# Kernel tuning notes

Hardware: AMD Instinct MI355X
Metric: run time of the kernel (lower is better)

The kernel has to match this reference:

```python
import jax, jax.numpy as jnp
import numpy as np

DIM = 768
H = 12          # num_heads
KV = 4          # kv_heads
D = DIM // H    # head_dim = 64
ROPE_BASE = 10000.0
WINDOW = 8
B, N = 4, 1024


def setup_inputs() -> dict:
    key = jax.random.key(0)
    ks = jax.random.split(key, 8)
    s = 0.02  # weight scale for sane magnitudes
    return {
        "x": jax.random.normal(ks[0], (B, N, DIM), jnp.float32),
        "Wq": jax.random.normal(ks[1], (2 * DIM, DIM), jnp.float32) * s,
        "Wk": jax.random.normal(ks[2], (2 * DIM * KV // H, DIM), jnp.float32) * s,
        "Wv1": jax.random.normal(ks[3], (DIM * KV // H, DIM), jnp.float32) * s,
        "Wv2": jax.random.normal(ks[4], (DIM * KV // H, DIM), jnp.float32) * s,
        "lambda_p": jnp.full((H, 1, 1), -2.0, jnp.float32),
        "Wo": jax.random.normal(ks[5], (DIM, DIM), jnp.float32) * s,
        "bo": jax.random.normal(ks[6], (DIM,), jnp.float32) * s,
    }


def _rotate_half(x):
    x1 = x[..., ::2]
    x2 = x[..., 1::2]
    return jnp.stack([-x2, x1], axis=-1).reshape(x.shape)


def _rope_cos_sin(n, dtype):
    side = int(n ** 0.5)
    if side * side == n:
        h = np.arange(side, dtype=np.float32)
        gh, gw = np.meshgrid(h, h, indexing="ij")
        pos_h, pos_w = gh.reshape(-1), gw.reshape(-1)
    else:
        pos_h = np.arange(n, dtype=np.float32)
        pos_w = np.zeros_like(pos_h)
    dim_half = D // 2
    inv_freq = ROPE_BASE ** (-np.arange(dim_half, dtype=np.float32) / dim_half)
    theta = np.concatenate([pos_h[:, None] * inv_freq[None, :],
                            pos_w[:, None] * inv_freq[None, :]], axis=1)  # [N, D]
    cos = jnp.asarray(np.cos(theta), dtype)[None, None]  # [1,1,N,D]
    sin = jnp.asarray(np.sin(theta), dtype)[None, None]
    return cos, sin


def _apply_rope(q, cos, sin):
    return q * cos + _rotate_half(q) * sin


def _qk_norm(t):
    return t / (jnp.linalg.norm(t, axis=-1, keepdims=True) + 1e-6)


def _window_mask(n, dtype):
    side = int(n ** 0.5)
    if side * side == n:
        h = np.arange(side)
        gh, gw = np.meshgrid(h, h, indexing="ij")
        coords = np.stack([gh.reshape(-1), gw.reshape(-1)], axis=1)  # [N,2]
        dist = np.abs(coords[:, None, :] - coords[None, :, :]).max(-1)  # Chebyshev
    else:
        idx = np.arange(n)
        dist = np.abs(idx[None, :] - idx[:, None])
    return jnp.asarray(np.where(dist > WINDOW, -np.inf, 0.0).astype(np.float32), dtype)


def _attend(q, k, v, mask):
    # q,k,v: [B,H,N,D]; mask additive [N,N]
    scale = 1.0 / np.sqrt(D)
    scores = jnp.einsum("bhnd,bhmd->bhnm", q, k) * scale + mask
    return jnp.einsum("bhnm,bhmd->bhnd", jax.nn.softmax(scores, axis=-1), v)


def reference(x, Wq, Wk, Wv1, Wv2, lambda_p, Wo, bo):
    b, n, c = x.shape
    rep = H // KV
    q = (x @ Wq.T).reshape(b, n, 2, H, D).transpose(2, 0, 3, 1, 4)   # [2,B,H,N,D]
    k = (x @ Wk.T).reshape(b, n, 2, KV, D).transpose(2, 0, 3, 1, 4)  # [2,B,KV,N,D]
    v1 = (x @ Wv1.T).reshape(b, n, KV, D).transpose(0, 2, 1, 3)      # [B,KV,N,D]
    v2 = (x @ Wv2.T).reshape(b, n, KV, D).transpose(0, 2, 1, 3)
    q1, q2 = q[0], q[1]
    k1, k2 = k[0], k[1]
    # GQA: repeat_interleave over head axis
    k1 = jnp.repeat(k1, rep, axis=1)
    k2 = jnp.repeat(k2, rep, axis=1)
    v1 = jnp.repeat(v1, rep, axis=1)
    v2 = jnp.repeat(v2, rep, axis=1)
    cos, sin = _rope_cos_sin(n, x.dtype)
    q1, q2 = _apply_rope(q1, cos, sin), _apply_rope(q2, cos, sin)
    k1, k2 = _apply_rope(k1, cos, sin), _apply_rope(k2, cos, sin)
    q1, q2, k1, k2 = _qk_norm(q1), _qk_norm(q2), _qk_norm(k1), _qk_norm(k2)
    mask = _window_mask(n, x.dtype)
    out1 = _attend(q1, k1, v1, mask)
    out2 = _attend(q2, k2, v2, mask)
    lam = jax.nn.softplus(lambda_p)  # [H,1,1] broadcasts over [B,H,N,D]
    out = out1 - lam[None] * out2
    out = out.transpose(0, 2, 1, 3).reshape(b, n, c)
    return out @ Wo.T + bo
```

## Files before the change

kernel.cpp:

```cpp
#include <hip/hip_runtime.h>
#include <hip/hip_bf16.h>

#define BATCH 4
#define NSEQ  1024
#define DIM   768
#define NH    12
#define NKV   4
#define HD    64
#define NTOK  (BATCH*NSEQ)

using bf16 = __hip_bfloat16;
typedef __attribute__((ext_vector_type(8))) short short8;
typedef __attribute__((ext_vector_type(4))) float floatx4;
typedef __attribute__((ext_vector_type(4))) unsigned uint4v;

__device__ __forceinline__ float b2f(short x) {
  unsigned u = ((unsigned)(unsigned short)x) << 16;
  return __builtin_bit_cast(float, u);
}
__device__ __forceinline__ unsigned short f2b(float f) {
  unsigned u = __builtin_bit_cast(unsigned, f);
  unsigned r = u + 0x7FFF + ((u >> 16) & 1);
  return (unsigned short)(r >> 16);
}
__device__ __forceinline__ unsigned cvtpk(float lo, float hi) {
  unsigned r;
  asm("v_cvt_pk_bf16_f32 %0, %1, %2" : "=v"(r) : "v"(lo), "v"(hi));
  return r;
}

__device__ __forceinline__ void load_lds_16(const bf16* g, bf16* l) {
  __builtin_amdgcn_global_load_lds(
      (const __attribute__((address_space(1))) void*)g,
      (__attribute__((address_space(3))) void*)l, 16, 0, 0);
}

__global__ __launch_bounds__(256) void cvt_all(
    const float* __restrict__ x,  const float* __restrict__ wq,
    const float* __restrict__ wk, const float* __restrict__ wv1,
    const float* __restrict__ wv2, const float* __restrict__ wo,
    bf16* __restrict__ xb,  bf16* __restrict__ wqb, bf16* __restrict__ wkb,
    bf16* __restrict__ wv1b, bf16* __restrict__ wv2b, bf16* __restrict__ wob)
{
  int i = blockIdx.x * 256 + threadIdx.x;
  const float* s; bf16* d; int off;
  if      (i <  786432) { s = x;   d = xb;   off = i; }
  else if (i < 1081344) { s = wq;  d = wqb;  off = i -  786432; }
  else if (i < 1179648) { s = wk;  d = wkb;  off = i - 1081344; }
  else if (i < 1228800) { s = wv1; d = wv1b; off = i - 1179648; }
  else if (i < 1277952) { s = wv2; d = wv2b; off = i - 1228800; }
  else                  { s = wo;  d = wob;  off = i - 1277952; }
  float4 f = reinterpret_cast<const float4*>(s)[off];
  ushort4 u;
  u.x = f2b(f.x); u.y = f2b(f.y); u.z = f2b(f.z); u.w = f2b(f.w);
  reinterpret_cast<ushort4*>(d)[off] = u;
}

__global__ __launch_bounds__(256, 2) void gemm_qkv(
    const bf16* __restrict__ xb,
    const bf16* __restrict__ Wqb, const bf16* __restrict__ Wkb,
    const bf16* __restrict__ Wv1b, const bf16* __restrict__ Wv2b,
    bf16* __restrict__ Qpk, bf16* __restrict__ Kpk,
    bf16* __restrict__ Vpk1, bf16* __restrict__ Vpk2)
{
  __shared__ __align__(16) bf16 As[128 * 64];
  __shared__ __align__(16) bf16 Ws[128 * 64];

  const int bn = blockIdx.x, bm = blockIdx.y;
  const bf16* Wp;
  if (bn < 12)      Wp = Wqb  + (size_t)bn * 128 * 768;
  else if (bn < 16) Wp = Wkb  + (size_t)(bn - 12) * 128 * 768;
  else if (bn < 18) Wp = Wv1b + (size_t)(bn - 16) * 128 * 768;
  else              Wp = Wv2b + (size_t)(bn - 18) * 128 * 768;

  const int t = threadIdx.x, wave = t >> 6, lane = t & 63;
  const int wm = wave >> 1, wn = wave & 1;
  const int quad = lane >> 4, lr = lane & 15;

  const int srow = wave * 32 + (lane >> 3);
  const int scol = ((lane & 7) ^ (lane >> 3)) * 8;
  const bf16* Ag = xb + (size_t)(bm * 128 + srow) * 768 + scol;
  const bf16* Wg = Wp + (size_t)srow * 768 + scol;
  bf16* Al = As + wave * 32 * 64;
  bf16* Wl = Ws + wave * 32 * 64;

  floatx4 acc[4][4] = {};

  for (int k0 = 0; k0 < 768; k0 += 64) {
    #pragma unroll
    for (int c = 0; c < 4; ++c) {
      load_lds_16(Ag + (size_t)c * 8 * 768 + k0, Al + c * 8 * 64);
      load_lds_16(Wg + (size_t)c * 8 * 768 + k0, Wl + c * 8 * 64);
    }
    __syncthreads();

    short8 af[4][2], wf[4][2];
    #pragma unroll
    for (int mt = 0; mt < 4; ++mt)
      #pragma unroll
      for (int ks = 0; ks < 2; ++ks)
        af[mt][ks] = *reinterpret_cast<const short8*>(
            &As[(wm * 64 + mt * 16 + lr) * 64 + ((ks * 32 + quad * 8) ^ ((lr & 7) * 8))]);
    #pragma unroll
    for (int nt = 0; nt < 4; ++nt)
      #pragma unroll
      for (int ks = 0; ks < 2; ++ks)
        wf[nt][ks] = *reinterpret_cast<const short8*>(
            &Ws[(wn * 64 + nt * 16 + lr) * 64 + ((ks * 32 + quad * 8) ^ ((lr & 7) * 8))]);

    #pragma unroll
    for (int mt = 0; mt < 4; ++mt)
      #pragma unroll
      for (int nt = 0; nt < 4; ++nt) {
        acc[mt][nt] = __builtin_amdgcn_mfma_f32_16x16x32_bf16(af[mt][0], wf[nt][0], acc[mt][nt], 0, 0, 0);
        acc[mt][nt] = __builtin_amdgcn_mfma_f32_16x16x32_bf16(af[mt][1], wf[nt][1], acc[mt][nt], 0, 0, 0);
      }
    __syncthreads();
  }

  if (bn < 16) {
    const float K2 = 0.41524101186098309f;
    const float invf0 = exp2f(-(float)lr * K2);
    const float invf1 = exp2f(-(float)(16 + lr) * K2);
    const float sgn = (lr & 1) ? 1.f : -1.f;
    const bool isq = (bn < 12);
    const int hq = bn * 2 + wn;
    const int sq_ = hq / 12, hq_ = hq % 12;
    const int hh = (bn - 12) * 2 + wn;
    const int sk_ = hh >> 2, kvh_ = hh & 3;
    const int qk128 = (lr >> 3) * 128;
    #pragma unroll
    for (int mt = 0; mt < 4; ++mt) {
      const int row0 = bm * 128 + wm * 64 + mt * 16 + quad * 4;
      const int n0 = row0 & (NSEQ - 1);
      const int bb = row0 >> 10, kh = n0 >> 5;
      const float ph = (float)kh;
      const float pw0 = (float)(n0 & 31);
      const float t0 = ph * invf0, t1 = ph * invf1;
      const float c0 = __cosf(t0), s0 = __sinf(t0);
      const float c1 = __cosf(t1), s1 = __sinf(t1);
      bf16* tb0;
      if (isq) {
        tb0 = Qpk + ((size_t)((bb * 2 + sq_) * 12 + hq_) * 32 + kh) * 2048
              + (size_t)(mt & 1) * 1024 + qk128 + (quad * 4) * 8 + (lr & 7);
      } else {
        tb0 = Kpk + ((size_t)((bb * 2 + sk_) * 4 + kvh_) * 32 + kh) * 2048
              + (size_t)(mt & 1) * 1024 + qk128 + (quad * 4) * 8 + (lr & 7);
      }
      #pragma unroll
      for (int r = 0; r < 4; ++r) {
        float v0 = acc[mt][0][r];
        float v1 = acc[mt][1][r];
        float v2 = acc[mt][2][r];
        float v3 = acc[mt][3][r];
        float rot0 = sgn * __shfl_xor(v0, 1);
        float rot1 = sgn * __shfl_xor(v1, 1);
        float rot2 = sgn * __shfl_xor(v2, 1);
        float rot3 = sgn * __shfl_xor(v3, 1);
        float pw = pw0 + (float)r;
        float t2 = pw * invf0, t3 = pw * invf1;
        float rv0 = v0 * c0 + rot0 * s0;
        float rv1 = v1 * c1 + rot1 * s1;
        float rv2 = v2 * __cosf(t2) + rot2 * __sinf(t2);
        float rv3 = v3 * __cosf(t3) + rot3 * __sinf(t3);
        float ss = rv0 * rv0 + rv1 * rv1 + rv2 * rv2 + rv3 * rv3;
        #pragma unroll
        for (int off = 1; off < 16; off <<= 1) ss += __shfl_xor(ss, off);
        float sc = 1.f / (sqrtf(ss) + 1e-6f);
        if (isq) sc *= 0.18033688011112042f;
        bf16* tb = tb0 + r * 8;
        unsigned pkA = cvtpk(rv0 * sc, rv1 * sc);
        unsigned pkB = cvtpk(rv2 * sc, rv3 * sc);
        *(unsigned short*)&tb[0]   = (unsigned short)pkA;
        *(unsigned short*)&tb[256] = (unsigned short)(pkA >> 16);
        *(unsigned short*)&tb[512] = (unsigned short)pkB;
        *(unsigned short*)&tb[768] = (unsigned short)(pkB >> 16);
      }
    }
  } else {
    const bool is2 = (bn >= 18);
    bf16* Vp = is2 ? Vpk2 : Vpk1;
    const int kvh_ = (bn - (is2 ? 18 : 16)) * 2 + wn;
    #pragma unroll
    for (int mt = 0; mt < 4; ++mt)
      #pragma unroll
      for (int r = 0; r < 4; ++r) {
        int row = bm * 128 + wm * 64 + mt * 16 + quad * 4 + r;
        int n = row & (NSEQ - 1);
        int bb = row >> 10, kh = n >> 5;
        int rowm = (mt & 1) * 16 + quad * 4 + r;
        int quad_v = rowm >> 3, j = rowm & 7;
        bf16* tb = Vp + ((size_t)(bb * 4 + kvh_) * 32 + kh) * 2048
                   + quad_v * 128 + lr * 8 + j;
        unsigned pkA = cvtpk(acc[mt][0][r], acc[mt][1][r]);
        unsigned pkB = cvtpk(acc[mt][2][r], acc[mt][3][r]);
        *(unsigned short*)&tb[0]    = (unsigned short)pkA;
        *(unsigned short*)&tb[512]  = (unsigned short)(pkA >> 16);
        *(unsigned short*)&tb[1024] = (unsigned short)pkB;
        *(unsigned short*)&tb[1536] = (unsigned short)(pkB >> 16);
      }
  }
}

__global__ __launch_bounds__(256) void gemm_out(
    const bf16* __restrict__ Xb, const bf16* __restrict__ Wob,
    float* __restrict__ out, const float* __restrict__ bias)
{
  __shared__ __align__(16) bf16 As[64 * 64];
  __shared__ __align__(16) bf16 Ws[64 * 64];

  const int bn = blockIdx.x, bm = blockIdx.y;
  const int t = threadIdx.x, wave = t >> 6, lane = t & 63;
  const int wm = wave >> 1, wn = wave & 1;
  const int quad = lane >> 4, lr = lane & 15;

  const int srow = wave * 16 + (lane >> 3);
  const int scol = ((lane & 7) ^ (lane >> 3)) * 8;
  const bf16* Ag = Xb  + (size_t)(bm * 64 + srow) * 768 + scol;
  const bf16* Wg = Wob + (size_t)(bn * 64 + srow) * 768 + scol;
  bf16* Al = As + wave * 16 * 64;
  bf16* Wl = Ws + wave * 16 * 64;

  floatx4 acc[2][2] = {};

  for (int k0 = 0; k0 < 768; k0 += 64) {
    #pragma unroll
    for (int c = 0; c < 2; ++c) {
      load_lds_16(Ag + (size_t)c * 8 * 768 + k0, Al + c * 8 * 64);
      load_lds_16(Wg + (size_t)c * 8 * 768 + k0, Wl + c * 8 * 64);
    }
    __syncthreads();

    short8 af[2][2], wf[2][2];
    #pragma unroll
    for (int mt = 0; mt < 2; ++mt)
      #pragma unroll
      for (int ks = 0; ks < 2; ++ks)
        af[mt][ks] = *reinterpret_cast<const short8*>(
            &As[(wm * 32 + mt * 16 + lr) * 64 + ((ks * 32 + quad * 8) ^ ((lr & 7) * 8))]);
    #pragma unroll
    for (int nt = 0; nt < 2; ++nt)
      #pragma unroll
      for (int ks = 0; ks < 2; ++ks)
        wf[nt][ks] = *reinterpret_cast<const short8*>(
            &Ws[(wn * 32 + nt * 16 + lr) * 64 + ((ks * 32 + quad * 8) ^ ((lr & 7) * 8))]);

    #pragma unroll
    for (int mt = 0; mt < 2; ++mt)
      #pragma unroll
      for (int nt = 0; nt < 2; ++nt) {
        acc[mt][nt] = __builtin_amdgcn_mfma_f32_16x16x32_bf16(af[mt][0], wf[nt][0], acc[mt][nt], 0, 0, 0);
        acc[mt][nt] = __builtin_amdgcn_mfma_f32_16x16x32_bf16(af[mt][1], wf[nt][1], acc[mt][nt], 0, 0, 0);
      }
    __syncthreads();
  }

  #pragma unroll
  for (int nt = 0; nt < 2; ++nt) {
    int col = bn * 64 + wn * 32 + nt * 16 + lr;
    float bv = bias[col];
    #pragma unroll
    for (int mt = 0; mt < 2; ++mt)
      #pragma unroll
      for (int r = 0; r < 4; ++r) {
        int row = bm * 64 + wm * 32 + mt * 16 + quad * 4 + r;
        out[(size_t)row * 768 + col] = acc[mt][nt][r] + bv;
      }
  }
}

struct Frag { short8 kf[2][2]; short8 vf[4]; };

__device__ __forceinline__ void attn_load(
    Frag& f, const bf16* __restrict__ kp, const bf16* __restrict__ vp,
    int kh, int lane8)
{
  const bf16* kt = kp + (size_t)kh * 2048 + lane8;
  const bf16* vt = vp + (size_t)kh * 2048 + lane8;
  f.kf[0][0] = *reinterpret_cast<const short8*>(kt);
  f.kf[0][1] = *reinterpret_cast<const short8*>(kt + 512);
  f.kf[1][0] = *reinterpret_cast<const short8*>(kt + 1024);
  f.kf[1][1] = *reinterpret_cast<const short8*>(kt + 1536);
  f.vf[0] = *reinterpret_cast<const short8*>(vt);
  f.vf[1] = *reinterpret_cast<const short8*>(vt + 512);
  f.vf[2] = *reinterpret_cast<const short8*>(vt + 1024);
  f.vf[3] = *reinterpret_cast<const short8*>(vt + 1536);
}

__device__ __forceinline__ void attn_step(
    const short8 (&qf)[2][2], const Frag& f, unsigned maskbits,
    floatx4 (&O)[2][4], float (&psum)[2], int quad)
{
  floatx4 St[2][2] = {};
  #pragma unroll
  for (int ks = 0; ks < 2; ++ks) {
    St[0][0] = __builtin_amdgcn_mfma_f32_16x16x32_bf16(f.kf[0][ks], qf[0][ks], St[0][0], 0, 0, 0);
    St[0][1] = __builtin_amdgcn_mfma_f32_16x16x32_bf16(f.kf[0][ks], qf[1][ks], St[0][1], 0, 0, 0);
    St[1][0] = __builtin_amdgcn_mfma_f32_16x16x32_bf16(f.kf[1][ks], qf[0][ks], St[1][0], 0, 0, 0);
    St[1][1] = __builtin_amdgcn_mfma_f32_16x16x32_bf16(f.kf[1][ks], qf[1][ks], St[1][1], 0, 0, 0);
  }

  unsigned pk[2][2][2];
  #pragma unroll
  for (int kt = 0; kt < 2; ++kt)
    #pragma unroll
    for (int mt = 0; mt < 2; ++mt) {
      float pr[4];
      #pragma unroll
      for (int r = 0; r < 4; ++r) {
        float p = __builtin_amdgcn_exp2f(St[kt][mt][r]);
        p = ((maskbits >> (kt * 8 + mt * 4 + r)) & 1u) ? p : 0.0f;
        psum[mt] += p;
        pr[r] = p;
      }
      pk[kt][mt][0] = cvtpk(pr[0], pr[1]);
      pk[kt][mt][1] = cvtpk(pr[2], pr[3]);
    }

  const bool oddq = (quad & 1);
  #pragma unroll
  for (int mt = 0; mt < 2; ++mt) {
    uint4v regs;
    #pragma unroll
    for (int h = 0; h < 2; ++h) {
      unsigned a = pk[0][mt][h], b = pk[1][mt][h];
      asm("v_permlane32_swap_b32 %0, %1" : "+v"(a), "+v"(b));
      unsigned sa = (unsigned)__shfl_xor((int)a, 16);
      unsigned sb = (unsigned)__shfl_xor((int)b, 16);
      regs[0 + h] = oddq ? sb : a;
      regs[2 + h] = oddq ? b  : sa;
    }
    short8 pa = __builtin_bit_cast(short8, regs);
    #pragma unroll
    for (int ntd = 0; ntd < 4; ++ntd)
      O[mt][ntd] = __builtin_amdgcn_mfma_f32_16x16x32_bf16(pa, f.vf[ntd], O[mt][ntd], 0, 0, 0);
  }
}

__global__ __launch_bounds__(256, 2) void attn_mfma(
    const bf16* __restrict__ Qpk, const bf16* __restrict__ Kpk,
    const bf16* __restrict__ Vpk1, const bf16* __restrict__ Vpk2,
    const float* __restrict__ lambda_p, bf16* __restrict__ X)
{
  __shared__ __align__(16) char smem[20480];

  const int bid = blockIdx.x;
  const int qh = bid & 31;
  const int hb = bid >> 5;
  const int h  = hb % 12;
  const int b  = hb / 12;
  const int kvh = h / 3;

  const int t = threadIdx.x;
  const int w = t >> 6;
  const int s = w >> 1;
  const int half = w & 1;
  const int lane = t & 63;
  const int quad = lane >> 4, lr = lane & 15;
  const int lane8 = lane * 8;

  float* myO = (float*)(smem + (s ? 10240 : 0));
  float* myP = (float*)(smem + (s ? 10240 : 0) + 8192);
  bf16* Xs = (bf16*)smem;

  const int tok0 = b * NSEQ + qh * 32;

  short8 qf[2][2];
  {
    const bf16* qt = Qpk + ((size_t)((b * 2 + s) * 12 + h) * 32 + qh) * 2048 + lane8;
    qf[0][0] = *reinterpret_cast<const short8*>(qt);
    qf[0][1] = *reinterpret_cast<const short8*>(qt + 512);
    qf[1][0] = *reinterpret_cast<const short8*>(qt + 1024);
    qf[1][1] = *reinterpret_cast<const short8*>(qt + 1536);
  }

  unsigned maskbits = 0;
  #pragma unroll
  for (int kt = 0; kt < 2; ++kt)
    #pragma unroll
    for (int mt = 0; mt < 2; ++mt)
      #pragma unroll
      for (int r = 0; r < 4; ++r) {
        int wk = kt * 16 + quad * 4 + r;
        int wq = mt * 16 + lr;
        int d = wk - wq; if (d < 0) d = -d;
        if (d <= 8) maskbits |= 1u << (kt * 8 + mt * 4 + r);
      }

  floatx4 O[2][4] = {};
  float psum[2] = {};

  const int kh0 = (qh > 8) ? qh - 8 : 0;
  const int kh1 = (qh < 23) ? qh + 8 : 31;
  const int cnt = kh1 - kh0 + 1;
  const int cA = (cnt + 1) >> 1;
  const int khA = half ? kh0 + cA : kh0;
  const int khB = half ? kh1 : kh0 + cA - 1;

  const bf16* kpbase = Kpk + (size_t)((b * 2 + s) * 4 + kvh) * 32 * 2048;
  const bf16* vpbase = (s ? Vpk2 : Vpk1) + (size_t)(b * 4 + kvh) * 32 * 2048;

  Frag fA, fB;
  attn_load(fA, kpbase, vpbase, khA, lane8);
  attn_load(fB, kpbase, vpbase, (khA + 1 <= khB) ? khA + 1 : khB, lane8);

  int i = khA;
  while (true) {
    attn_step(qf, fA, maskbits, O, psum, quad);
    if (i == khB) break;
    ++i;
    attn_load(fA, kpbase, vpbase, (i + 1 <= khB) ? i + 1 : i, lane8);
    attn_step(qf, fB, maskbits, O, psum, quad);
    if (i == khB) break;
    ++i;
    attn_load(fB, kpbase, vpbase, (i + 1 <= khB) ? i + 1 : i, lane8);
  }

  auto writeslab = [&]() {
    #pragma unroll
    for (int mt = 0; mt < 2; ++mt)
      #pragma unroll
      for (int ntd = 0; ntd < 4; ++ntd)
        *reinterpret_cast<floatx4*>(&myO[(mt * 4 + ntd) * 256 + lane * 4]) = O[mt][ntd];
    myP[lane]      = psum[0];
    myP[64 + lane] = psum[1];
  };
  auto readadd_norm = [&]() {
    #pragma unroll
    for (int mt = 0; mt < 2; ++mt)
      #pragma unroll
      for (int ntd = 0; ntd < 4; ++ntd)
        O[mt][ntd] += *reinterpret_cast<const floatx4*>(&myO[(mt * 4 + ntd) * 256 + lane * 4]);
    psum[0] += myP[lane];
    psum[1] += myP[64 + lane];
    #pragma unroll
    for (int mt = 0; mt < 2; ++mt) {
      psum[mt] += __shfl_xor(psum[mt], 16);
      psum[mt] += __shfl_xor(psum[mt], 32);
      psum[mt] = 1.f / psum[mt];
    }
    #pragma unroll
    for (int mt = 0; mt < 2; ++mt) {
      float invq[4];
      #pragma unroll
      for (int r = 0; r < 4; ++r)
        invq[r] = __shfl(psum[mt], (lane & 48) + quad * 4 + r);
      #pragma unroll
      for (int ntd = 0; ntd < 4; ++ntd)
        #pragma unroll
        for (int r = 0; r < 4; ++r)
          O[mt][ntd][r] *= invq[r];
    }
  };

  __syncthreads();
  if (half) writeslab();
  __syncthreads();
  if (!half) {
    readadd_norm();
    if (s) {
      #pragma unroll
      for (int mt = 0; mt < 2; ++mt)
        #pragma unroll
        for (int ntd = 0; ntd < 4; ++ntd)
          *reinterpret_cast<floatx4*>(&myO[(mt * 4 + ntd) * 256 + lane * 4]) = O[mt][ntd];
    }
  }
  __syncthreads();
  if (w == 0) {
    const float* O2s = (const float*)(smem + 10240);
    float lam = log1pf(__expf(lambda_p[h]));
    #pragma unroll
    for (int mt = 0; mt < 2; ++mt)
      #pragma unroll
      for (int ntd = 0; ntd < 4; ++ntd) {
        floatx4 o2 = *reinterpret_cast<const floatx4*>(&O2s[(mt * 4 + ntd) * 256 + lane * 4]);
        #pragma unroll
        for (int r = 0; r < 4; ++r) {
          float xv = O[mt][ntd][r] - lam * o2[r];
          *(unsigned short*)&Xs[(mt * 16 + quad * 4 + r) * 72 + ntd * 16 + lr] = f2b(xv);
        }
      }
  }
  __syncthreads();

  {
    int row = t >> 3, seg = t & 7;
    short8 xv = *reinterpret_cast<const short8*>(&Xs[row * 72 + seg * 8]);
    *reinterpret_cast<short8*>(X + (size_t)(tok0 + row) * 768 + h * 64 + seg * 8) = xv;
  }
}

extern "C" void kernel_launch(void* const* d_in, const int* in_sizes, int n_in,
                              void* d_out, int out_size, void* d_ws, size_t ws_size,
                              hipStream_t stream)
{
  const float* x        = (const float*)d_in[0];
  const float* Wq       = (const float*)d_in[1];
  const float* Wk       = (const float*)d_in[2];
  const float* Wv1      = (const float*)d_in[3];
  const float* Wv2      = (const float*)d_in[4];
  const float* lambda_p = (const float*)d_in[5];
  const float* Wo       = (const float*)d_in[6];
  const float* bo       = (const float*)d_in[7];
  float* out = (float*)d_out;

  bf16* xb   = (bf16*)d_ws;
  bf16* Wqb  = xb   + (size_t)NTOK * 768;
  bf16* Wkb  = Wqb  + (size_t)1536 * 768;
  bf16* Wv1b = Wkb  + (size_t)512 * 768;
  bf16* Wv2b = Wv1b + (size_t)256 * 768;
  bf16* Wob  = Wv2b + (size_t)256 * 768;
  bf16* Qpk  = Wob  + (size_t)768 * 768;
  bf16* Xb   = Qpk  + (size_t)NTOK * 1536;
  bf16* Vpk1 = Xb   + (size_t)NTOK * 768;
  bf16* Vpk2 = Vpk1 + (size_t)512 * 2048;
  bf16* Kpk  = Vpk2 + (size_t)512 * 2048;

  cvt_all<<<5568, 256, 0, stream>>>(x, Wq, Wk, Wv1, Wv2, Wo,
                                    xb, Wqb, Wkb, Wv1b, Wv2b, Wob);

  gemm_qkv<<<dim3(20, 32), 256, 0, stream>>>(xb, Wqb, Wkb, Wv1b, Wv2b,
                                             Qpk, Kpk, Vpk1, Vpk2);

  attn_mfma<<<BATCH * NH * 32, 256, 0, stream>>>(Qpk, Kpk, Vpk1, Vpk2, lambda_p, Xb);

  gemm_out<<<dim3(12, 64), 256, 0, stream>>>(Xb, Wob, out, bo);
}
```

Baseline: 143.9 us.

## Permute packed V layout to drop P shuffles and fold mask into MFMA init

Changes the packed V write layout so the bf16 probability fragments produced by the QK MFMA can feed the PV MFMA directly. This removes the permlane32 swap, the shfl_xor and the selects per step. The mask is now applied by seeding the score accumulators with 0 or -1e38, so exp2 yields zero for masked entries, replacing the per-element bit test. The change depends on the producer GEMM's V layout and the attention consumer agreeing exactly, which couples the two kernels.

Result: no change. 145.0 us (+0.8%).

```diff
diff --git a/kernel.cpp b/kernel.cpp
--- a/kernel.cpp
+++ b/kernel.cpp
@@ -189,7 +189,8 @@
         int n = row & (NSEQ - 1);
         int bb = row >> 10, kh = n >> 5;
         int rowm = (mt & 1) * 16 + quad * 4 + r;
-        int quad_v = rowm >> 3, j = rowm & 7;
+        int quad_v = (rowm >> 2) & 3;
+        int j = ((rowm >> 4) << 2) | (rowm & 3);
         bf16* tb = Vp + ((size_t)(bb * 4 + kvh_) * 32 + kh) * 2048
                    + quad_v * 128 + lr * 8 + j;
         unsigned pkA = cvtpk(acc[mt][0][r], acc[mt][1][r]);
@@ -288,10 +289,10 @@
 }
 
 __device__ __forceinline__ void attn_step(
-    const short8 (&qf)[2][2], const Frag& f, unsigned maskbits,
-    floatx4 (&O)[2][4], float (&psum)[2], int quad)
-{
-  floatx4 St[2][2] = {};
+    const short8 (&qf)[2][2], const Frag& f, const floatx4 (&Sinit)[2][2],
+    floatx4 (&O)[2][4], float (&psum)[2])
+{
+  floatx4 St[2][2] = {{Sinit[0][0], Sinit[0][1]}, {Sinit[1][0], Sinit[1][1]}};
   #pragma unroll
   for (int ks = 0; ks < 2; ++ks) {
     St[0][0] = __builtin_amdgcn_mfma_f32_16x16x32_bf16(f.kf[0][ks], qf[0][ks], St[0][0], 0, 0, 0);
@@ -309,7 +310,6 @@
       #pragma unroll
       for (int r = 0; r < 4; ++r) {
         float p = __builtin_amdgcn_exp2f(St[kt][mt][r]);
-        p = ((maskbits >> (kt * 8 + mt * 4 + r)) & 1u) ? p : 0.0f;
         psum[mt] += p;
         pr[r] = p;
       }
@@ -317,19 +317,13 @@
       pk[kt][mt][1] = cvtpk(pr[2], pr[3]);
     }
 
-  const bool oddq = (quad & 1);
   #pragma unroll
   for (int mt = 0; mt < 2; ++mt) {
     uint4v regs;
-    #pragma unroll
-    for (int h = 0; h < 2; ++h) {
-      unsigned a = pk[0][mt][h], b = pk[1][mt][h];
-      asm("v_permlane32_swap_b32 %0, %1" : "+v"(a), "+v"(b));
-      unsigned sa = (unsigned)__shfl_xor((int)a, 16);
-      unsigned sb = (unsigned)__shfl_xor((int)b, 16);
-      regs[0 + h] = oddq ? sb : a;
-      regs[2 + h] = oddq ? b  : sa;
-    }
+    regs[0] = pk[0][mt][0];
+    regs[1] = pk[0][mt][1];
+    regs[2] = pk[1][mt][0];
+    regs[3] = pk[1][mt][1];
     short8 pa = __builtin_bit_cast(short8, regs);
     #pragma unroll
     for (int ntd = 0; ntd < 4; ++ntd)
@@ -374,7 +368,7 @@
     qf[1][1] = *reinterpret_cast<const short8*>(qt + 1536);
   }
 
-  unsigned maskbits = 0;
+  floatx4 Sinit[2][2];
   #pragma unroll
   for (int kt = 0; kt < 2; ++kt)
     #pragma unroll
@@ -384,7 +378,7 @@
         int wk = kt * 16 + quad * 4 + r;
         int wq = mt * 16 + lr;
         int d = wk - wq; if (d < 0) d = -d;
-        if (d <= 8) maskbits |= 1u << (kt * 8 + mt * 4 + r);
+        Sinit[kt][mt][r] = (d <= 8) ? 0.0f : -1e38f;
       }
 
   floatx4 O[2][4] = {};
@@ -406,11 +400,11 @@
 
   int i = khA;
   while (true) {
-    attn_step(qf, fA, maskbits, O, psum, quad);
+    attn_step(qf, fA, Sinit, O, psum);
     if (i == khB) break;
     ++i;
     attn_load(fA, kpbase, vpbase, (i + 1 <= khB) ? i + 1 : i, lane8);
-    attn_step(qf, fB, maskbits, O, psum, quad);
+    attn_step(qf, fB, Sinit, O, psum);
     if (i == khB) break;
     ++i;
     attn_load(fB, kpbase, vpbase, (i + 1 <= khB) ? i + 1 : i, lane8);
```
